# Performance work log

Measured on AMD Instinct MI355X. Metric: run time of the kernel, lower is better.

Reference implementation:

```python
import jax, jax.numpy as jnp
import numpy as np

D = 1024      # input_dim
H = 16        # head_num
HD = 64       # head_dim
HID = 4096    # mlp hidden
CUR = 512     # cur_seq
PREV = 512    # prev_seq (memory)
FULL = CUR + PREV
BS = 16
SCALE = 1.0 / (HD ** 0.5)


def setup_inputs() -> dict:
    key = jax.random.key(0)
    ks = jax.random.split(key, 20)
    def nrm(k, shape, s=0.02):
        return (jax.random.normal(k, shape) * s).astype(jnp.float32)
    inp = {
        "inputs": nrm(ks[0], (CUR, BS, D), 1.0),
        "pos_embedding": nrm(ks[1], (FULL, 1, D), 1.0),
        "u": nrm(ks[2], (H, HD)),
        "v": nrm(ks[3], (H, HD)),
        "memory": nrm(ks[4], (PREV, BS, D), 1.0),
        # causal mask: position i (query) may attend to j <= i + PREV; True = masked
        "mask": jnp.triu(jnp.ones((CUR, FULL), dtype=bool), k=PREV + 1)[:, :, None],
        # attention params (stored as (in, out); torch Linear applies x @ W.T + b)
        "Wkv": nrm(ks[5], (D, 2 * H * HD)), "bkv": jnp.zeros((2 * H * HD,), jnp.float32),
        "Wq": nrm(ks[6], (D, H * HD)), "bq": jnp.zeros((H * HD,), jnp.float32),
        "Wo": nrm(ks[7], (H * HD, D)), "bo": jnp.zeros((D,), jnp.float32),
        "Wp": nrm(ks[8], (D, H * HD)), "bp": jnp.zeros((H * HD,), jnp.float32),
        # layernorms
        "ln1_g": jnp.ones((D,), jnp.float32), "ln1_b": jnp.zeros((D,), jnp.float32),
        "ln2_g": jnp.ones((D,), jnp.float32), "ln2_b": jnp.zeros((D,), jnp.float32),
        # mlp (mlp_num=2): Linear(D,HID)+relu, Linear(HID,D)+relu
        "W1": nrm(ks[9], (D, HID)), "b1": jnp.zeros((HID,), jnp.float32),
        "W2": nrm(ks[10], (HID, D)), "b2": jnp.zeros((D,), jnp.float32),
        # GRU gates: stacked [Wr,Wz,Wg] and [Ur,Uz,Ug], no bias; bg init 2.0
        "g1_W": nrm(ks[11], (3, D, D)), "g1_U": nrm(ks[12], (3, D, D)),
        "g1_bg": jnp.full((D,), 2.0, jnp.float32),
        "g2_W": nrm(ks[13], (3, D, D)), "g2_U": nrm(ks[14], (3, D, D)),
        "g2_bg": jnp.full((D,), 2.0, jnp.float32),
    }
    return inp


def _layernorm(x, g, b, eps=1e-5):
    mu = jnp.mean(x, axis=-1, keepdims=True)
    var = jnp.mean(jnp.square(x - mu), axis=-1, keepdims=True)
    return (x - mu) * jax.lax.rsqrt(var + eps) * g + b


def _rel_shift(x):
    # x: (bs, head, cur, full) -> pad/reshape/slice trick of Transformer-XL
    b, h, c, f = x.shape
    xp = jnp.pad(x, ((0, 0), (0, 0), (0, 0), (1, 0)))      # (b,h,c,f+1)
    xp = xp.reshape(b, h, f + 1, c)
    return xp[:, :, 1:, :].reshape(b, h, c, f)


def _gru_gate(x, y, W, U, bg):
    # W, U: (3, D, D) for [r, z, g] gates; torch Linear => y @ W[i].T
    r = jax.nn.sigmoid(y @ W[0].T + x @ U[0].T)
    z = jax.nn.sigmoid(y @ W[1].T + x @ U[1].T - bg)
    h = jnp.tanh(y @ W[2].T + (r * x) @ U[2].T)
    return (1.0 - z) * x + z * h


def _attention_xl(x_cur, pos_emb, x_full, u, v, mask,
                  Wkv, bkv, Wq, bq, Wo, bo, Wp, bp):
    cur, bs, _ = x_cur.shape
    full = x_full.shape[0]
    kv = x_full @ Wkv + bkv                                  # (full, bs, 2*H*HD)
    key, value = jnp.split(kv, 2, axis=-1)
    query = x_cur @ Wq + bq                                  # (cur, bs, H*HD)
    r = (pos_emb @ Wp + bp).reshape(full, H, HD)             # (full, H, HD)

    key = key.reshape(full, bs, H, HD)
    value = value.reshape(full, bs, H, HD)
    query = query.reshape(cur, bs, H, HD)

    content = jnp.einsum('ibhd,jbhd->bhij', query + u, key)  # (bs,H,cur,full)
    position = jnp.einsum('ibhd,jhd->bhij', query + v, r)    # (bs,H,cur,full)
    position = _rel_shift(position)

    attn = (content + position) * SCALE
    # mask: (cur, full, 1) bool, True = masked
    m = mask[:, :, 0][None, None]                            # (1,1,cur,full)
    attn = jnp.where(m, -jnp.inf, attn)
    p = jax.nn.softmax(attn, axis=-1)

    out = jnp.einsum('bhij,jbhd->ibhd', p, value).reshape(cur, bs, H * HD)
    return out @ Wo + bo                                     # (cur, bs, D)


def reference(inputs, pos_embedding, u, v, memory, mask,
              Wkv, bkv, Wq, bq, Wo, bo, Wp, bp,
              ln1_g, ln1_b, ln2_g, ln2_b,
              W1, b1, W2, b2,
              g1_W, g1_U, g1_bg, g2_W, g2_U, g2_bg):
    prev = memory.shape[0]
    full_input = jnp.concatenate([memory, inputs], axis=0)   # (full, bs, D)
    x1 = _layernorm(full_input, ln1_g, ln1_b)
    a1 = _attention_xl(x1[prev:], pos_embedding, x1, u, v, mask,
                       Wkv, bkv, Wq, bq, Wo, bo, Wp, bp)
    a1 = jax.nn.relu(a1)                                     # dropout = identity (eval)
    o1 = _gru_gate(inputs, a1, g1_W, g1_U, g1_bg)
    x2 = _layernorm(o1, ln2_g, ln2_b)
    m2 = jax.nn.relu(jax.nn.relu(x2 @ W1 + b1) @ W2 + b2)    # mlp: act after every linear
    o2 = _gru_gate(o1, m2, g2_W, g2_U, g2_bg)
    return o2
```

## Files before the change

### kernel.cpp

```cpp
#include <hip/hip_runtime.h>
#include <stdint.h>

typedef _Float16 h16;
typedef __attribute__((ext_vector_type(8))) _Float16 f16x8;
typedef __attribute__((ext_vector_type(4))) _Float16 f16x4;
typedef __attribute__((ext_vector_type(4))) float f32x4;

enum { F_OBF = 1, F_BIAS = 2, F_RELU = 4, F_ACC = 8, F_DUAL = 16 };

static __device__ __forceinline__ void gload16(const void* g, void* l) {
  __builtin_amdgcn_global_load_lds((__attribute__((address_space(1))) void*)g,
                                   (__attribute__((address_space(3))) void*)l,
                                   16, 0, 0);
}

template <int BM, int BN, int WAVES_M, int WAVES_N, int FLAGS>
__global__ __launch_bounds__(256) void gemm_k(
    const h16* __restrict__ A, const h16* __restrict__ B,
    void* __restrict__ Cv, void* __restrict__ C2v,
    const float* __restrict__ bias, const float* __restrict__ bias2,
    int K, int lda, int ldb, int ldc,
    long sAb, long sAh, long sBb, long sBh, long sCb, long sCh) {
  constexpr int BK = 32;
  constexpr int WM = BM / WAVES_M, WN = BN / WAVES_N;
  constexpr int MF = WM / 16, NF = WN / 16;
  constexpr int LPS = BM / 64 + BN / 64;
  __shared__ h16 Al[3][BM][BK];
  __shared__ h16 Bl[3][BN][BK];

  const int tid = threadIdx.x, lane = tid & 63, wid = tid >> 6;
  const int wm = wid / WAVES_N, wn = wid % WAVES_N;
  const int z = blockIdx.z, zb = z >> 4, zh = z & 15;
  const h16* Ab = A + zb * sAb + zh * sAh + (long)blockIdx.x * BM * lda;
  const h16* Bb = B + zb * sBb + zh * sBh + (long)blockIdx.y * BN * ldb;

  const int srow = lane >> 2;
  const int skc = (((lane & 3) ^ ((lane >> 3) & 3)) * 8);

  auto stage = [&](int buf, int k0) {
#pragma unroll
    for (int t = 0; t < BM / 64; ++t) {
      const int ii = wid + t * 4;
      gload16(Ab + (long)(ii * 16 + srow) * lda + k0 + skc, &Al[buf][ii * 16][0]);
    }
#pragma unroll
    for (int t = 0; t < BN / 64; ++t) {
      const int ii = wid + t * 4;
      gload16(Bb + (long)(ii * 16 + srow) * ldb + k0 + skc, &Bl[buf][ii * 16][0]);
    }
  };

  f32x4 acc[MF][NF] = {};
  const int nk = K / BK;
  const int ar = lane & 15, ls = lane >> 4;

  stage(0, 0);
  if (nk > 1) stage(1, BK);
  for (int kt = 0; kt < nk; ++kt) {
    if (kt == nk - 1) {
      asm volatile("s_waitcnt vmcnt(0)" ::: "memory");
    } else if constexpr (LPS == 4) {
      asm volatile("s_waitcnt vmcnt(4)" ::: "memory");
    } else if constexpr (LPS == 3) {
      asm volatile("s_waitcnt vmcnt(3)" ::: "memory");
    } else {
      asm volatile("s_waitcnt vmcnt(0)" ::: "memory");
    }
    __builtin_amdgcn_s_barrier();
    asm volatile("" ::: "memory");
    if (kt + 2 < nk) stage((kt + 2) % 3, (kt + 2) * BK);
    const int cur = kt % 3;
    f16x8 af[MF], bv[NF];
#pragma unroll
    for (int m = 0; m < MF; ++m) {
      const int R = wm * WM + m * 16 + ar;
      af[m] = *(const f16x8*)&Al[cur][R][(ls ^ ((R >> 1) & 3)) * 8];
    }
#pragma unroll
    for (int n = 0; n < NF; ++n) {
      const int R = wn * WN + n * 16 + ar;
      bv[n] = *(const f16x8*)&Bl[cur][R][(ls ^ ((R >> 1) & 3)) * 8];
    }
#pragma unroll
    for (int m = 0; m < MF; ++m)
#pragma unroll
      for (int n = 0; n < NF; ++n)
        acc[m][n] = __builtin_amdgcn_mfma_f32_16x16x32_f16(af[m], bv[n], acc[m][n], 0, 0, 0);
  }

  const long coff = (long)zb * sCb + (long)zh * sCh;
#pragma unroll
  for (int m = 0; m < MF; ++m) {
#pragma unroll
    for (int n = 0; n < NF; ++n) {
      const int col = blockIdx.y * BN + wn * WN + n * 16 + ar;
      float bv1 = 0.f, bv2 = 0.f;
      if (FLAGS & F_BIAS) bv1 = bias[col];
      if (FLAGS & F_DUAL) bv2 = bias2[col];
#pragma unroll
      for (int r = 0; r < 4; ++r) {
        const int row = blockIdx.x * BM + wm * WM + m * 16 + (lane >> 4) * 4 + r;
        float val = acc[m][n][r] + bv1;
        if (FLAGS & F_RELU) val = fmaxf(val, 0.f);
        if constexpr ((FLAGS & F_ACC) != 0) {
          float* p = (float*)Cv + coff + (long)row * ldc + col;
          *p = *p + val;
        } else if constexpr ((FLAGS & F_OBF) != 0) {
          ((h16*)Cv)[coff + (long)row * ldc + col] = (h16)val;
          if constexpr ((FLAGS & F_DUAL) != 0)
            ((h16*)C2v)[coff + (long)row * ldc + col] = (h16)(acc[m][n][r] + bv2);
        } else {
          ((float*)Cv)[coff + (long)row * ldc + col] = val;
        }
      }
    }
  }
}

__global__ __launch_bounds__(256) void fattn_k(
    const h16* __restrict__ qu, const h16* __restrict__ qv,
    const h16* __restrict__ kvb, const h16* __restrict__ vT,
    const h16* __restrict__ rb, h16* __restrict__ attn) {
  __shared__ h16 Kl[128][64];
  __shared__ h16 Vl[64][128];
  __shared__ h16 Psc[4][16][164];

  const int tid = threadIdx.x, lane = tid & 63, wv = tid >> 6;
  const int z = blockIdx.x, b = z >> 4, h = z & 15;
  const int i0 = blockIdx.y * 64;
  const int ar = lane & 15, q4 = lane >> 4;
  const int myrow = i0 + wv * 16;

  const long qoff = ((long)(myrow + ar) * 16 + b) * 1024 + h * 64 + q4 * 8;
  f16x8 quf[2], qvf[2];
  quf[0] = *(const f16x8*)&qu[qoff];
  quf[1] = *(const f16x8*)&qu[qoff + 32];
  qvf[0] = *(const f16x8*)&qv[qoff];
  qvf[1] = *(const f16x8*)&qv[qoff + 32];

  f32x4 o[4] = {};
  float mrow[4], lrow[4];
#pragma unroll
  for (int r = 0; r < 4; ++r) { mrow[r] = -3e38f; lrow[r] = 0.f; }

  const int ntiles = (i0 + 575 + 128) >> 7;

  for (int t = 0; t < ntiles; ++t) {
    const int j0 = t * 128;
    __builtin_amdgcn_s_barrier();
#pragma unroll
    for (int it = 0; it < 4; ++it) {
      const int ch = it * 256 + wv * 64 + lane;
      const int kr = ch >> 3, ks = ch & 7;
      gload16(kvb + ((long)(j0 + kr) * 16 + b) * 2048 + h * 64 + (ks ^ (kr & 7)) * 8,
              (char*)&Kl[0][0] + (it * 256 + wv * 64) * 16);
    }
#pragma unroll
    for (int it = 0; it < 4; ++it) {
      const int ch = it * 256 + wv * 64 + lane;
      const int vd = ch >> 4, vs = ch & 15;
      gload16(vT + ((long)z * 64 + vd) * 1024 + j0 + (vs ^ (vd & 7)) * 8,
              (char*)&Vl[0][0] + (it * 256 + wv * 64) * 16);
    }
    asm volatile("s_waitcnt vmcnt(0)" ::: "memory");
    __builtin_amdgcn_s_barrier();

    f32x4 acc_c[8] = {};
#pragma unroll
    for (int kd = 0; kd < 2; ++kd)
#pragma unroll
      for (int nf = 0; nf < 8; ++nf) {
        const int j = nf * 16 + ar;
        const int phys = (kd * 4 + q4) ^ (j & 7);
        const f16x8 kf = *(const f16x8*)&Kl[j][phys * 8];
        acc_c[nf] = __builtin_amdgcn_mfma_f32_16x16x32_f16(quf[kd], kf, acc_c[nf], 0, 0, 0);
      }

    const int jbase = j0 - myrow + 496;
    f32x4 acc_p[9] = {};
#pragma unroll
    for (int kd = 0; kd < 2; ++kd)
#pragma unroll
      for (int jf = 0; jf < 9; ++jf) {
        int jjr = jbase + jf * 16 + ar;
        if (jjr > 1023) jjr = 1023;
        const f16x8 rf = *(const f16x8*)&rb[(long)jjr * 1024 + h * 64 + kd * 32 + q4 * 8];
        acc_p[jf] = __builtin_amdgcn_mfma_f32_16x16x32_f16(qvf[kd], rf, acc_p[jf], 0, 0, 0);
      }
#pragma unroll
    for (int jf = 0; jf < 9; ++jf)
#pragma unroll
      for (int r = 0; r < 4; ++r)
        Psc[wv][q4 * 4 + r][jf * 16 + ar] = (h16)acc_p[jf][r];

    float p[8][4];
#pragma unroll
    for (int nf = 0; nf < 8; ++nf)
#pragma unroll
      for (int r = 0; r < 4; ++r) {
        const int iloc = q4 * 4 + r;
        const int jloc = nf * 16 + ar;
        const int band = jloc - iloc + 15;
        const float pv = (float)Psc[wv][iloc][band];
        float sv = (acc_c[nf][r] + pv) * 0.125f;
        const bool ok = (j0 + jloc) <= (myrow + iloc + 512);
        p[nf][r] = ok ? sv : -3e38f;
      }
#pragma unroll
    for (int r = 0; r < 4; ++r) {
      float tm = -3e38f;
#pragma unroll
      for (int nf = 0; nf < 8; ++nf) tm = fmaxf(tm, p[nf][r]);
      tm = fmaxf(tm, __shfl_xor(tm, 1));
      tm = fmaxf(tm, __shfl_xor(tm, 2));
      tm = fmaxf(tm, __shfl_xor(tm, 4));
      tm = fmaxf(tm, __shfl_xor(tm, 8));
      const float mn = fmaxf(mrow[r], tm);
      const float sc = __expf(mrow[r] - mn);
      mrow[r] = mn;
      float ts = 0.f;
#pragma unroll
      for (int nf = 0; nf < 8; ++nf) {
        const float e = __expf(p[nf][r] - mn);
        p[nf][r] = e;
        ts += e;
      }
      ts += __shfl_xor(ts, 1);
      ts += __shfl_xor(ts, 2);
      ts += __shfl_xor(ts, 4);
      ts += __shfl_xor(ts, 8);
      lrow[r] = lrow[r] * sc + ts;
#pragma unroll
      for (int v = 0; v < 4; ++v) o[v][r] *= sc;
    }

#pragma unroll
    for (int nf = 0; nf < 8; ++nf)
#pragma unroll
      for (int r = 0; r < 4; ++r) {
        const int iloc = q4 * 4 + r, jloc = nf * 16 + ar;
        Psc[wv][iloc][((jloc >> 3) ^ (iloc & 7)) * 8 + (jloc & 7)] = (h16)p[nf][r];
      }
#pragma unroll
    for (int ks = 0; ks < 4; ++ks) {
      const f16x8 pa = *(const f16x8*)&Psc[wv][ar][((ks * 4 + q4) ^ (ar & 7)) * 8];
#pragma unroll
      for (int vnf = 0; vnf < 4; ++vnf) {
        const int d = vnf * 16 + ar;
        const f16x8 vb = *(const f16x8*)&Vl[d][((ks * 4 + q4) ^ (d & 7)) * 8];
        o[vnf] = __builtin_amdgcn_mfma_f32_16x16x32_f16(pa, vb, o[vnf], 0, 0, 0);
      }
    }
  }

#pragma unroll
  for (int vnf = 0; vnf < 4; ++vnf)
#pragma unroll
    for (int r = 0; r < 4; ++r) {
      const int i_ = myrow + q4 * 4 + r;
      attn[((long)i_ * 16 + b) * 1024 + h * 64 + vnf * 16 + ar] =
          (h16)(o[vnf][r] / lrow[r]);
    }
}

__global__ __launch_bounds__(256) void wtrans_k(const float* __restrict__ in,
                                                h16* __restrict__ out, int K, int N) {
  __shared__ float t[32][33];
  const int tx = threadIdx.x & 31, ty = threadIdx.x >> 5;
  const int n0 = blockIdx.x * 32, k0 = blockIdx.y * 32;
#pragma unroll
  for (int j = 0; j < 32; j += 8)
    t[ty + j][tx] = in[(long)(k0 + ty + j) * N + n0 + tx];
  __syncthreads();
#pragma unroll
  for (int j = 0; j < 32; j += 8)
    out[(long)(n0 + ty + j) * K + k0 + tx] = (h16)t[tx][ty + j];
}

__global__ __launch_bounds__(256) void cast_k(const float* __restrict__ in,
                                              h16* __restrict__ out, long n4) {
  const long i = (long)blockIdx.x * 256 + threadIdx.x;
  if (i >= n4) return;
  const float4 v = ((const float4*)in)[i];
  f16x4 o;
  o[0] = (h16)v.x; o[1] = (h16)v.y; o[2] = (h16)v.z; o[3] = (h16)v.w;
  ((f16x4*)out)[i] = o;
}

__global__ void addbias_k(const float* __restrict__ bq, const float* __restrict__ u,
                          const float* __restrict__ v, float* __restrict__ qu,
                          float* __restrict__ qv) {
  const int c = blockIdx.x * 256 + threadIdx.x;
  if (c < 1024) { qu[c] = bq[c] + u[c]; qv[c] = bq[c] + v[c]; }
}

__global__ __launch_bounds__(256) void zero_out_k(float* __restrict__ out, long n) {
  const long i = (long)blockIdx.x * 256 + threadIdx.x;
  if (i < n) out[i] = 0.f;
}

__global__ __launch_bounds__(256) void ln_k(const float* __restrict__ src0,
                                            const float* __restrict__ src1, int rows0,
                                            const float* __restrict__ g,
                                            const float* __restrict__ b,
                                            h16* __restrict__ out) {
  const int row = blockIdx.x, tid = threadIdx.x;
  const float* src = (row < rows0) ? (src0 + (long)row * 1024)
                                   : (src1 + (long)(row - rows0) * 1024);
  const float4 x = ((const float4*)src)[tid];
  float s = x.x + x.y + x.z + x.w;
  float sq = x.x * x.x + x.y * x.y + x.z * x.z + x.w * x.w;
#pragma unroll
  for (int o = 32; o > 0; o >>= 1) { s += __shfl_down(s, o); sq += __shfl_down(sq, o); }
  __shared__ float red[8];
  const int lane = tid & 63, w = tid >> 6;
  if (lane == 0) { red[w] = s; red[4 + w] = sq; }
  __syncthreads();
  s = red[0] + red[1] + red[2] + red[3];
  sq = red[4] + red[5] + red[6] + red[7];
  const float mu = s * (1.f / 1024.f);
  const float inv = rsqrtf(sq * (1.f / 1024.f) - mu * mu + 1e-5f);
  const float4 gg = ((const float4*)g)[tid], bb = ((const float4*)b)[tid];
  f16x4 o;
  o[0] = (h16)((x.x - mu) * inv * gg.x + bb.x);
  o[1] = (h16)((x.y - mu) * inv * gg.y + bb.y);
  o[2] = (h16)((x.z - mu) * inv * gg.z + bb.z);
  o[3] = (h16)((x.w - mu) * inv * gg.w + bb.w);
  ((f16x4*)(out + (long)row * 1024))[tid] = o;
}

__global__ __launch_bounds__(256) void vtrans_k(const h16* __restrict__ kv,
                                                h16* __restrict__ vT) {
  const int z = blockIdx.y, b = z >> 4, h = z & 15;
  const int j0 = blockIdx.x * 64;
  __shared__ h16 t[64][72];
  const int jj = threadIdx.x >> 3, c = threadIdx.x & 7;
#pragma unroll
  for (int half = 0; half < 2; ++half) {
    const int j = jj + half * 32;
    const f16x8 v = *(const f16x8*)(kv + ((long)(j0 + j) * 16 + b) * 2048 + 1024 + h * 64 + c * 8);
    *(f16x8*)&t[j][c * 8] = v;
  }
  __syncthreads();
#pragma unroll
  for (int half = 0; half < 2; ++half) {
    const int d = jj + half * 32;
    f16x8 o;
#pragma unroll
    for (int k = 0; k < 8; ++k) o[k] = t[c * 8 + k][d];
    *(f16x8*)(vT + ((long)z * 64 + d) * 1024 + j0 + c * 8) = o;
  }
}

__global__ __launch_bounds__(256) void gru_rx_k(const float* __restrict__ T,
                                                const float* __restrict__ x,
                                                h16* __restrict__ rx) {
  const long i = (long)blockIdx.x * 256 + threadIdx.x;
  const long row = i >> 8;
  const int c4 = (int)(i & 255);
  const float4 t = *((const float4*)(T + row * 3072) + c4);
  const float4 xx = ((const float4*)x)[i];
  f16x4 o;
  o[0] = (h16)(xx.x / (1.f + __expf(-t.x)));
  o[1] = (h16)(xx.y / (1.f + __expf(-t.y)));
  o[2] = (h16)(xx.z / (1.f + __expf(-t.z)));
  o[3] = (h16)(xx.w / (1.f + __expf(-t.w)));
  ((f16x4*)rx)[i] = o;
}

__global__ __launch_bounds__(256) void gru_out_k(const float* __restrict__ T,
                                                 const float* __restrict__ x,
                                                 const float* __restrict__ bg,
                                                 float* __restrict__ outf,
                                                 h16* __restrict__ outh) {
  const long i = (long)blockIdx.x * 256 + threadIdx.x;
  const long row = i >> 8;
  const int c4 = (int)(i & 255);
  const float4 tz = *((const float4*)(T + row * 3072 + 1024) + c4);
  const float4 th = *((const float4*)(T + row * 3072 + 2048) + c4);
  const float4 xx = ((const float4*)x)[i];
  const float4 bb = ((const float4*)bg)[c4];
  float4 o;
  {
    const float z0 = 1.f / (1.f + __expf(-(tz.x - bb.x)));
    const float z1 = 1.f / (1.f + __expf(-(tz.y - bb.y)));
    const float z2 = 1.f / (1.f + __expf(-(tz.z - bb.z)));
    const float z3 = 1.f / (1.f + __expf(-(tz.w - bb.w)));
    o.x = (1.f - z0) * xx.x + z0 * tanhf(th.x);
    o.y = (1.f - z1) * xx.y + z1 * tanhf(th.y);
    o.z = (1.f - z2) * xx.z + z2 * tanhf(th.z);
    o.w = (1.f - z3) * xx.w + z3 * tanhf(th.w);
  }
  ((float4*)outf)[i] = o;
  if (outh != nullptr) {
    f16x4 oh;
    oh[0] = (h16)o.x; oh[1] = (h16)o.y; oh[2] = (h16)o.z; oh[3] = (h16)o.w;
    ((f16x4*)outh)[i] = oh;
  }
}

extern "C" void kernel_launch(void* const* d_in, const int* in_sizes, int n_in,
                              void* d_out, int out_size, void* d_ws, size_t ws_size,
                              hipStream_t stream) {
  const float* inputs = (const float*)d_in[0];
  const float* pos    = (const float*)d_in[1];
  const float* u      = (const float*)d_in[2];
  const float* v      = (const float*)d_in[3];
  const float* memory = (const float*)d_in[4];
  const float* Wkv = (const float*)d_in[6];  const float* bkv = (const float*)d_in[7];
  const float* Wq  = (const float*)d_in[8];  const float* bq  = (const float*)d_in[9];
  const float* Wo  = (const float*)d_in[10]; const float* bo  = (const float*)d_in[11];
  const float* Wp  = (const float*)d_in[12]; const float* bp  = (const float*)d_in[13];
  const float* ln1_g = (const float*)d_in[14]; const float* ln1_b = (const float*)d_in[15];
  const float* ln2_g = (const float*)d_in[16]; const float* ln2_b = (const float*)d_in[17];
  const float* W1 = (const float*)d_in[18]; const float* b1 = (const float*)d_in[19];
  const float* W2 = (const float*)d_in[20]; const float* b2 = (const float*)d_in[21];
  const float* g1_W = (const float*)d_in[22]; const float* g1_U = (const float*)d_in[23];
  const float* g1_bg = (const float*)d_in[24];
  const float* g2_W = (const float*)d_in[25]; const float* g2_U = (const float*)d_in[26];
  const float* g2_bg = (const float*)d_in[27];
  (void)in_sizes; (void)n_in;

  const size_t MB = 1u << 20;
  const size_t NEEDED = 247 * MB;
  const dim3 blk(256);
  if (ws_size < NEEDED) {
    zero_out_k<<<(out_size + 255) / 256, blk, 0, stream>>>((float*)d_out, out_size);
    return;
  }

  char* w = (char*)d_ws;
  h16* WoT   = (h16*)(w + 0 * MB);
  h16* W1T   = (h16*)(w + 2 * MB);
  h16* W2T   = (h16*)(w + 10 * MB);
  h16* g1Wb  = (h16*)(w + 18 * MB);
  h16* g1Ub  = (h16*)(w + 24 * MB);
  h16* g2Wb  = (h16*)(w + 30 * MB);
  h16* g2Ub  = (h16*)(w + 36 * MB);
  h16* WkvT  = (h16*)(w + 42 * MB);
  h16* WqT   = (h16*)(w + 46 * MB);
  h16* WpT   = (h16*)(w + 48 * MB);
  h16* posb  = (h16*)(w + 50 * MB);
  float* bias_qu = (float*)(w + 52 * MB);
  float* bias_qv = (float*)(w + 52 * MB + 8192);
  h16* xb    = (h16*)(w + 53 * MB);
  h16* x1    = (h16*)(w + 69 * MB);
  char* Rbig =        w + 101 * MB;
  h16* qu    = (h16*)(w + 197 * MB);
  h16* qv    = (h16*)(w + 213 * MB);
  h16* rb    = (h16*)(w + 229 * MB);
  h16* attn  = (h16*)(w + 231 * MB);

  h16*   kvb  = (h16*)Rbig;
  float* Tall = (float*)Rbig;
  h16*   h1   = (h16*)Rbig;
  h16*   vT   = x1;
  h16*   a1   = qu;
  h16*   rx1  = qv;
  float* o1f  = (float*)qu;
  h16*   o1b  = attn;
  h16*   x2   = x1;
  h16*   m2   = x1 + 8L * 1024 * 1024;
  h16*   rx2  = x1;

  wtrans_k<<<dim3(64, 32), blk, 0, stream>>>(Wkv, WkvT, 1024, 2048);
  wtrans_k<<<dim3(32, 32), blk, 0, stream>>>(Wq, WqT, 1024, 1024);
  wtrans_k<<<dim3(32, 32), blk, 0, stream>>>(Wo, WoT, 1024, 1024);
  wtrans_k<<<dim3(32, 32), blk, 0, stream>>>(Wp, WpT, 1024, 1024);
  wtrans_k<<<dim3(128, 32), blk, 0, stream>>>(W1, W1T, 1024, 4096);
  wtrans_k<<<dim3(32, 128), blk, 0, stream>>>(W2, W2T, 4096, 1024);
  cast_k<<<3072, blk, 0, stream>>>(g1_W, g1Wb, 786432);
  cast_k<<<3072, blk, 0, stream>>>(g1_U, g1Ub, 786432);
  cast_k<<<3072, blk, 0, stream>>>(g2_W, g2Wb, 786432);
  cast_k<<<3072, blk, 0, stream>>>(g2_U, g2Ub, 786432);
  cast_k<<<1024, blk, 0, stream>>>(pos, posb, 262144);
  cast_k<<<8192, blk, 0, stream>>>(inputs, xb, 2097152);
  addbias_k<<<4, blk, 0, stream>>>(bq, u, v, bias_qu, bias_qv);

  ln_k<<<16384, blk, 0, stream>>>(memory, inputs, 8192, ln1_g, ln1_b, x1);

  gemm_k<128, 128, 2, 2, F_OBF | F_BIAS><<<dim3(128, 16, 1), blk, 0, stream>>>(
      x1, WkvT, kvb, nullptr, bkv, nullptr, 1024, 1024, 1024, 2048, 0, 0, 0, 0, 0, 0);
  gemm_k<64, 128, 2, 2, F_OBF | F_BIAS | F_DUAL><<<dim3(128, 8, 1), blk, 0, stream>>>(
      x1 + 8192L * 1024, WqT, qu, qv, bias_qu, bias_qv, 1024, 1024, 1024, 1024, 0, 0, 0, 0, 0, 0);
  gemm_k<128, 128, 2, 2, F_OBF | F_BIAS><<<dim3(8, 8, 1), blk, 0, stream>>>(
      posb, WpT, rb, nullptr, bp, nullptr, 1024, 1024, 1024, 1024, 0, 0, 0, 0, 0, 0);
  vtrans_k<<<dim3(16, 256), blk, 0, stream>>>(kvb, vT);

  fattn_k<<<dim3(256, 8), blk, 0, stream>>>(qu, qv, kvb, vT, rb, attn);

  gemm_k<64, 128, 2, 2, F_OBF | F_BIAS | F_RELU><<<dim3(128, 8, 1), blk, 0, stream>>>(
      attn, WoT, a1, nullptr, bo, nullptr, 1024, 1024, 1024, 1024, 0, 0, 0, 0, 0, 0);

  gemm_k<128, 128, 2, 2, 0><<<dim3(64, 24, 1), blk, 0, stream>>>(
      a1, g1Wb, Tall, nullptr, nullptr, nullptr, 1024, 1024, 1024, 3072, 0, 0, 0, 0, 0, 0);
  gemm_k<128, 128, 2, 2, F_ACC><<<dim3(64, 16, 1), blk, 0, stream>>>(
      xb, g1Ub, Tall, nullptr, nullptr, nullptr, 1024, 1024, 1024, 3072, 0, 0, 0, 0, 0, 0);
  gru_rx_k<<<8192, blk, 0, stream>>>(Tall, inputs, rx1);
  gemm_k<64, 128, 2, 2, F_ACC><<<dim3(128, 8, 1), blk, 0, stream>>>(
      rx1, g1Ub + 2L * 1024 * 1024, Tall + 2048, nullptr, nullptr, nullptr,
      1024, 1024, 1024, 3072, 0, 0, 0, 0, 0, 0);
  gru_out_k<<<8192, blk, 0, stream>>>(Tall, inputs, g1_bg, o1f, o1b);

  ln_k<<<8192, blk, 0, stream>>>(o1f, o1f, 8192, ln2_g, ln2_b, x2);
  gemm_k<128, 128, 2, 2, F_OBF | F_BIAS | F_RELU><<<dim3(64, 32, 1), blk, 0, stream>>>(
      x2, W1T, h1, nullptr, b1, nullptr, 1024, 1024, 1024, 4096, 0, 0, 0, 0, 0, 0);
  gemm_k<64, 128, 2, 2, F_OBF | F_BIAS | F_RELU><<<dim3(128, 8, 1), blk, 0, stream>>>(
      h1, W2T, m2, nullptr, b2, nullptr, 4096, 4096, 4096, 1024, 0, 0, 0, 0, 0, 0);

  gemm_k<128, 128, 2, 2, 0><<<dim3(64, 24, 1), blk, 0, stream>>>(
      m2, g2Wb, Tall, nullptr, nullptr, nullptr, 1024, 1024, 1024, 3072, 0, 0, 0, 0, 0, 0);
  gemm_k<128, 128, 2, 2, F_ACC><<<dim3(64, 16, 1), blk, 0, stream>>>(
      o1b, g2Ub, Tall, nullptr, nullptr, nullptr, 1024, 1024, 1024, 3072, 0, 0, 0, 0, 0, 0);
  gru_rx_k<<<8192, blk, 0, stream>>>(Tall, o1f, rx2);
  gemm_k<64, 128, 2, 2, F_ACC><<<dim3(128, 8, 1), blk, 0, stream>>>(
      rx2, g2Ub + 2L * 1024 * 1024, Tall + 2048, nullptr, nullptr, nullptr,
      1024, 1024, 1024, 3072, 0, 0, 0, 0, 0, 0);
  gru_out_k<<<8192, blk, 0, stream>>>(Tall, o1f, g2_bg, (float*)d_out, nullptr);
}
```

Measured before the change: 1.191 ms.

## Add 256x256-tile 8-wave GEMM kernel for the large projection GEMMs

Result: faster. 1.133 ms (-4.9%).

```diff
diff --git a/kernel.cpp b/kernel.cpp
--- a/kernel.cpp
+++ b/kernel.cpp
@@ -8,10 +8,177 @@
 
 enum { F_OBF = 1, F_BIAS = 2, F_RELU = 4, F_ACC = 8, F_DUAL = 16 };
 
+#define BARRIER_MEM                                  \
+  do {                                               \
+    asm volatile("" ::: "memory");                   \
+    __builtin_amdgcn_s_barrier();                    \
+    asm volatile("" ::: "memory");                   \
+  } while (0)
+
 static __device__ __forceinline__ void gload16(const void* g, void* l) {
   __builtin_amdgcn_global_load_lds((__attribute__((address_space(1))) void*)g,
                                    (__attribute__((address_space(3))) void*)l,
                                    16, 0, 0);
+}
+
+template <int FLAGS>
+__global__ __launch_bounds__(512) void gemm2_k(
+    const h16* __restrict__ A, const h16* __restrict__ B,
+    void* __restrict__ Cv, const float* __restrict__ bias,
+    int K, int lda, int ldb, int ldc, int gm) {
+  __shared__ h16 Al[2][256][64];
+  __shared__ h16 Bl[2][256][64];
+
+  const int tid = threadIdx.x, lane = tid & 63, wid = tid >> 6;
+  const int wr = wid >> 2, wn = wid & 3;
+  const int ar = lane & 15, q4 = lane >> 4;
+
+  const int nwg = gridDim.x, cpx = nwg >> 3;
+  const int bid = (blockIdx.x & 7) * cpx + (blockIdx.x >> 3);
+  const int mx = bid % gm, ny = bid / gm;
+
+  const h16* Ab = A + (long)mx * 256 * lda;
+  const h16* Bb = B + (long)ny * 256 * ldb;
+
+  auto stageA = [&](int buf, int half, int k0) {
+#pragma unroll
+    for (int l = 0; l < 2; ++l) {
+      const int idx = l * 512 + tid;
+      const int row = half * 128 + (idx >> 3), sl = idx & 7;
+      gload16(Ab + (long)row * lda + k0 + (sl ^ (row & 7)) * 8,
+              (char*)&Al[buf][0][0] + (half * 1024 + l * 512 + wid * 64) * 16);
+    }
+  };
+  auto stageB = [&](int buf, int half, int k0) {
+#pragma unroll
+    for (int l = 0; l < 2; ++l) {
+      const int idx = l * 512 + tid;
+      const int row = half * 128 + (idx >> 3), sl = idx & 7;
+      gload16(Bb + (long)row * ldb + k0 + (sl ^ (row & 7)) * 8,
+              (char*)&Bl[buf][0][0] + (half * 1024 + l * 512 + wid * 64) * 16);
+    }
+  };
+
+  f32x4 acc[8][4] = {};
+  const int nk = K >> 6;
+
+  stageB(0, 0, 0); stageB(0, 1, 0); stageA(0, 0, 0); stageA(0, 1, 0);
+  if (nk > 1) { stageB(1, 0, 64); stageB(1, 1, 64); stageA(1, 0, 64); stageA(1, 1, 64); }
+  if (nk > 1) asm volatile("s_waitcnt vmcnt(8)" ::: "memory");
+  else        asm volatile("s_waitcnt vmcnt(0)" ::: "memory");
+  BARRIER_MEM;
+
+  for (int kt = 0; kt < nk; ++kt) {
+    const int b = kt & 1;
+    const int k2 = (kt + 2) << 6;
+    const bool pf = (kt + 2) < nk;
+
+    f16x8 a0[4][2], b0[2][2];
+#pragma unroll
+    for (int m = 0; m < 4; ++m) {
+      const int row = wr * 128 + m * 16 + ar;
+#pragma unroll
+      for (int ks = 0; ks < 2; ++ks)
+        a0[m][ks] = *(const f16x8*)&Al[b][row][((ks * 4 + q4) ^ (row & 7)) * 8];
+    }
+#pragma unroll
+    for (int n = 0; n < 2; ++n) {
+      const int row = wn * 64 + n * 16 + ar;
+#pragma unroll
+      for (int ks = 0; ks < 2; ++ks)
+        b0[n][ks] = *(const f16x8*)&Bl[b][row][((ks * 4 + q4) ^ (row & 7)) * 8];
+    }
+    BARRIER_MEM;
+    __builtin_amdgcn_s_setprio(1);
+#pragma unroll
+    for (int m = 0; m < 4; ++m)
+#pragma unroll
+      for (int n = 0; n < 2; ++n)
+#pragma unroll
+        for (int ks = 0; ks < 2; ++ks)
+          acc[m][n] = __builtin_amdgcn_mfma_f32_16x16x32_f16(a0[m][ks], b0[n][ks], acc[m][n], 0, 0, 0);
+    __builtin_amdgcn_s_setprio(0);
+    BARRIER_MEM;
+
+    f16x8 b1f[2][2];
+#pragma unroll
+    for (int n = 0; n < 2; ++n) {
+      const int row = wn * 64 + (n + 2) * 16 + ar;
+#pragma unroll
+      for (int ks = 0; ks < 2; ++ks)
+        b1f[n][ks] = *(const f16x8*)&Bl[b][row][((ks * 4 + q4) ^ (row & 7)) * 8];
+    }
+    BARRIER_MEM;
+    __builtin_amdgcn_s_setprio(1);
+#pragma unroll
+    for (int m = 0; m < 4; ++m)
+#pragma unroll
+      for (int n = 0; n < 2; ++n)
+#pragma unroll
+        for (int ks = 0; ks < 2; ++ks)
+          acc[m][n + 2] = __builtin_amdgcn_mfma_f32_16x16x32_f16(a0[m][ks], b1f[n][ks], acc[m][n + 2], 0, 0, 0);
+    __builtin_amdgcn_s_setprio(0);
+    BARRIER_MEM;
+
+    f16x8 a1f[4][2];
+#pragma unroll
+    for (int m = 0; m < 4; ++m) {
+      const int row = wr * 128 + (m + 4) * 16 + ar;
+#pragma unroll
+      for (int ks = 0; ks < 2; ++ks)
+        a1f[m][ks] = *(const f16x8*)&Al[b][row][((ks * 4 + q4) ^ (row & 7)) * 8];
+    }
+    if (pf) { stageB(b, 0, k2); stageB(b, 1, k2); }
+    BARRIER_MEM;
+    __builtin_amdgcn_s_setprio(1);
+#pragma unroll
+    for (int m = 0; m < 4; ++m)
+#pragma unroll
+      for (int n = 0; n < 2; ++n)
+#pragma unroll
+        for (int ks = 0; ks < 2; ++ks)
+          acc[m + 4][n] = __builtin_amdgcn_mfma_f32_16x16x32_f16(a1f[m][ks], b0[n][ks], acc[m + 4][n], 0, 0, 0);
+    __builtin_amdgcn_s_setprio(0);
+    BARRIER_MEM;
+
+    if (pf) { stageA(b, 0, k2); stageA(b, 1, k2); }
+    __builtin_amdgcn_s_setprio(1);
+#pragma unroll
+    for (int m = 0; m < 4; ++m)
+#pragma unroll
+      for (int n = 0; n < 2; ++n)
+#pragma unroll
+        for (int ks = 0; ks < 2; ++ks)
+          acc[m + 4][n + 2] = __builtin_amdgcn_mfma_f32_16x16x32_f16(a1f[m][ks], b1f[n][ks], acc[m + 4][n + 2], 0, 0, 0);
+    __builtin_amdgcn_s_setprio(0);
+    if (pf)                 asm volatile("s_waitcnt vmcnt(8)" ::: "memory");
+    else if (kt + 1 < nk)   asm volatile("s_waitcnt vmcnt(0)" ::: "memory");
+    BARRIER_MEM;
+  }
+
+#pragma unroll
+  for (int m = 0; m < 8; ++m) {
+#pragma unroll
+    for (int n = 0; n < 4; ++n) {
+      const int col = ny * 256 + wn * 64 + n * 16 + ar;
+      float bv1 = 0.f;
+      if (FLAGS & F_BIAS) bv1 = bias[col];
+#pragma unroll
+      for (int r = 0; r < 4; ++r) {
+        const int row = mx * 256 + wr * 128 + m * 16 + q4 * 4 + r;
+        float val = acc[m][n][r] + bv1;
+        if (FLAGS & F_RELU) val = fmaxf(val, 0.f);
+        if constexpr ((FLAGS & F_ACC) != 0) {
+          float* p = (float*)Cv + (long)row * ldc + col;
+          *p = *p + val;
+        } else if constexpr ((FLAGS & F_OBF) != 0) {
+          ((h16*)Cv)[(long)row * ldc + col] = (h16)val;
+        } else {
+          ((float*)Cv)[(long)row * ldc + col] = val;
+        }
+      }
+    }
+  }
 }
 
 template <int BM, int BN, int WAVES_M, int WAVES_N, int FLAGS>
@@ -479,8 +646,8 @@
 
   ln_k<<<16384, blk, 0, stream>>>(memory, inputs, 8192, ln1_g, ln1_b, x1);
 
-  gemm_k<128, 128, 2, 2, F_OBF | F_BIAS><<<dim3(128, 16, 1), blk, 0, stream>>>(
-      x1, WkvT, kvb, nullptr, bkv, nullptr, 1024, 1024, 1024, 2048, 0, 0, 0, 0, 0, 0);
+  gemm2_k<F_OBF | F_BIAS><<<dim3(512), dim3(512), 0, stream>>>(
+      x1, WkvT, kvb, bkv, 1024, 1024, 1024, 2048, 64);
   gemm_k<64, 128, 2, 2, F_OBF | F_BIAS | F_DUAL><<<dim3(128, 8, 1), blk, 0, stream>>>(
       x1 + 8192L * 1024, WqT, qu, qv, bias_qu, bias_qv, 1024, 1024, 1024, 1024, 0, 0, 0, 0, 0, 0);
   gemm_k<128, 128, 2, 2, F_OBF | F_BIAS><<<dim3(8, 8, 1), blk, 0, stream>>>(
@@ -492,10 +659,10 @@
   gemm_k<64, 128, 2, 2, F_OBF | F_BIAS | F_RELU><<<dim3(128, 8, 1), blk, 0, stream>>>(
       attn, WoT, a1, nullptr, bo, nullptr, 1024, 1024, 1024, 1024, 0, 0, 0, 0, 0, 0);
 
-  gemm_k<128, 128, 2, 2, 0><<<dim3(64, 24, 1), blk, 0, stream>>>(
-      a1, g1Wb, Tall, nullptr, nullptr, nullptr, 1024, 1024, 1024, 3072, 0, 0, 0, 0, 0, 0);
-  gemm_k<128, 128, 2, 2, F_ACC><<<dim3(64, 16, 1), blk, 0, stream>>>(
-      xb, g1Ub, Tall, nullptr, nullptr, nullptr, 1024, 1024, 1024, 3072, 0, 0, 0, 0, 0, 0);
+  gemm2_k<0><<<dim3(384), dim3(512), 0, stream>>>(
+      a1, g1Wb, Tall, nullptr, 1024, 1024, 1024, 3072, 32);
+  gemm2_k<F_ACC><<<dim3(256), dim3(512), 0, stream>>>(
+      xb, g1Ub, Tall, nullptr, 1024, 1024, 1024, 3072, 32);
   gru_rx_k<<<8192, blk, 0, stream>>>(Tall, inputs, rx1);
   gemm_k<64, 128, 2, 2, F_ACC><<<dim3(128, 8, 1), blk, 0, stream>>>(
       rx1, g1Ub + 2L * 1024 * 1024, Tall + 2048, nullptr, nullptr, nullptr,
@@ -503,15 +670,15 @@
   gru_out_k<<<8192, blk, 0, stream>>>(Tall, inputs, g1_bg, o1f, o1b);
 
   ln_k<<<8192, blk, 0, stream>>>(o1f, o1f, 8192, ln2_g, ln2_b, x2);
-  gemm_k<128, 128, 2, 2, F_OBF | F_BIAS | F_RELU><<<dim3(64, 32, 1), blk, 0, stream>>>(
-      x2, W1T, h1, nullptr, b1, nullptr, 1024, 1024, 1024, 4096, 0, 0, 0, 0, 0, 0);
+  gemm2_k<F_OBF | F_BIAS | F_RELU><<<dim3(512), dim3(512), 0, stream>>>(
+      x2, W1T, h1, b1, 1024, 1024, 1024, 4096, 32);
   gemm_k<64, 128, 2, 2, F_OBF | F_BIAS | F_RELU><<<dim3(128, 8, 1), blk, 0, stream>>>(
       h1, W2T, m2, nullptr, b2, nullptr, 4096, 4096, 4096, 1024, 0, 0, 0, 0, 0, 0);
 
-  gemm_k<128, 128, 2, 2, 0><<<dim3(64, 24, 1), blk, 0, stream>>>(
-      m2, g2Wb, Tall, nullptr, nullptr, nullptr, 1024, 1024, 1024, 3072, 0, 0, 0, 0, 0, 0);
-  gemm_k<128, 128, 2, 2, F_ACC><<<dim3(64, 16, 1), blk, 0, stream>>>(
-      o1b, g2Ub, Tall, nullptr, nullptr, nullptr, 1024, 1024, 1024, 3072, 0, 0, 0, 0, 0, 0);
+  gemm2_k<0><<<dim3(384), dim3(512), 0, stream>>>(
+      m2, g2Wb, Tall, nullptr, 1024, 1024, 1024, 3072, 32);
+  gemm2_k<F_ACC><<<dim3(256), dim3(512), 0, stream>>>(
+      o1b, g2Ub, Tall, nullptr, 1024, 1024, 1024, 3072, 32);
   gru_rx_k<<<8192, blk, 0, stream>>>(Tall, o1f, rx2);
   gemm_k<64, 128, 2, 2, F_ACC><<<dim3(128, 8, 1), blk, 0, stream>>>(
       rx2, g2Ub + 2L * 1024 * 1024, Tall + 2048, nullptr, nullptr, nullptr,
```
